# Optimization experiments

Measured on AMD Instinct MI355X. Metric: run time of the kernel, lower is better.

Reference implementation:

```python
import jax, jax.numpy as jnp
import numpy as np

L = 2048          # memory_length
NB = 512          # attn_num_basis
HID = 1024        # n_heads * head_dim
H = 16            # n_heads
D = 64            # head_dim
B = 8             # batch
QLEN = 2048
RIDGE = 0.5
SIGMAS = np.array([0.005, 0.01], dtype=np.float64)


def _build_basis_and_G():
    # torch.meshgrid(linspace(0,1,NB//2), sigmas) with 'ij' indexing, then flatten:
    mu_lin = np.linspace(0.0, 1.0, NB // len(SIGMAS))
    basis_mu = np.repeat(mu_lin, len(SIGMAS))          # [NB]
    basis_sigma = np.tile(SIGMAS, NB // len(SIGMAS))   # [NB]
    # get_positions with padding, even memory_length:
    shift = 1.0 / (2.0 * L)
    pos = np.linspace(-0.5 + shift, 1.5 - shift, 2 * L)  # [2L]
    # F[j, p] = N(pos_p; mu_j, sigma_j^2)
    F = np.exp(-0.5 * ((pos[None, :] - basis_mu[:, None]) / basis_sigma[:, None]) ** 2) \
        / (basis_sigma[:, None] * np.sqrt(2.0 * np.pi))  # [NB, 2L]
    G = F.T @ np.linalg.inv(F @ F.T + RIDGE * np.eye(NB))  # [2L, NB]
    Gs = G[L // 2: -(L // 2)]                              # [L, NB]
    return (basis_mu.astype(np.float32), basis_sigma.astype(np.float32),
            Gs.astype(np.float32))


def setup_inputs() -> dict:
    key = jax.random.key(0)
    ks = jax.random.split(key, 10)
    basis_mu, basis_sigma, Gs = _build_basis_and_G()
    inp = {
        "k": jax.random.normal(ks[0], (B, L, HID), jnp.float32),
        "query": jax.random.normal(ks[1], (B, H, QLEN, D), jnp.float32),
        "W_mask": jax.random.normal(ks[2], (L, L), jnp.float32) * (L ** -0.5),
        "b_mask": jnp.zeros((L,), jnp.float32),
        "Wq": jax.random.normal(ks[3], (HID, HID), jnp.float32) * (HID ** -0.5),
        "Wk": jax.random.normal(ks[4], (HID, HID), jnp.float32) * (HID ** -0.5),
        "Wv": jax.random.normal(ks[5], (HID, HID), jnp.float32) * (HID ** -0.5),
        "Wo": jax.random.normal(ks[6], (HID, HID), jnp.float32) * (HID ** -0.5),
        "w_mu": jax.random.normal(ks[7], (NB,), jnp.float32) * (NB ** -0.5),
        "w_sigma": jax.random.normal(ks[8], (NB,), jnp.float32) * (NB ** -0.5),
        "Gs": jnp.asarray(Gs),
        "basis_mu": jnp.asarray(basis_mu),
        "basis_sigma": jnp.asarray(basis_sigma),
    }
    return inp


def reference(k, query, W_mask, b_mask, Wq, Wk, Wv, Wo, w_mu, w_sigma,
              Gs, basis_mu, basis_sigma):
    b, l, hid = k.shape
    _, h, q, d = query.shape
    # k -> [B, hid, L]; affine mask over memory-length dim + sigmoid gate
    km = jnp.swapaxes(k, 1, 2)
    reg_mask = jax.nn.sigmoid(jnp.einsum('bhl,ml->bhm', km, W_mask) + b_mask)
    km = km * reg_mask
    # value_function: B = (k @ Gs).permute(0,2,1) -> [B, NB, hid]
    Bmat = jnp.einsum('bhl,ln->bnh', km, Gs)
    keys = (Bmat @ Wk.T).reshape(b, -1, h, d).transpose(0, 2, 1, 3)   # [B,H,NB,d]
    vals = (Bmat @ Wv.T).reshape(b, -1, h, d).transpose(0, 2, 1, 3)   # [B,H,NB,d]
    qh = (query.transpose(0, 2, 1, 3).reshape(b, q, hid) @ Wq.T)
    qh = qh.reshape(b, q, h, d).transpose(0, 2, 1, 3)                 # [B,H,q,d]
    # score: q / sqrt(head_dim) @ keys^T -> [B,H,q,NB]
    scores = jnp.einsum('bhqd,bhnd->bhqn', qh / jnp.sqrt(jnp.float32(d)), keys)
    # affine mu / sigma^2 of the continuous attention Gaussian
    mu = jax.nn.sigmoid(scores @ w_mu)[..., None]                      # [B,H,q,1]
    sigma_sq = jnp.maximum(jax.nn.softplus(scores @ w_sigma), 1e-6)[..., None]
    # ContinuousSoftmax with Gaussian basis: r_j = E_{t~N(mu,sig^2)}[psi_j(t)]
    #                                            = N(mu_j; mu, sig^2 + sigma_j^2)
    var = sigma_sq + basis_sigma ** 2                                  # [B,H,q,NB]
    r = jnp.exp(-0.5 * (mu - basis_mu) ** 2 / var) / jnp.sqrt(2.0 * jnp.pi * var)
    ctx = jnp.einsum('bhqn,bhnd->bqhd', r, vals).reshape(b, q, hid)
    return ctx @ Wo.T
```

## Files before the change

### kernel.cpp

```cpp
#include <hip/hip_runtime.h>
#include <hip/hip_bf16.h>

#define L_   2048
#define NB_  512
#define HID_ 1024
#define H_   16
#define D_   64
#define B_   8
#define Q_   2048

typedef unsigned short u16;
typedef float  f32x4  __attribute__((ext_vector_type(4)));
typedef short  short8 __attribute__((ext_vector_type(8)));

__device__ __forceinline__ u16 f2b_e22(float x) {
    __hip_bfloat16 h = __float2bfloat16(x);
    union { __hip_bfloat16 h; u16 u; } cv; cv.h = h; return cv.u;
}
__device__ __forceinline__ float b2f_e22(u16 u) {
    union { u16 u; __hip_bfloat16 h; } cv; cv.u = u; return __bfloat162float(cv.h);
}
__device__ __forceinline__ float ldin_e22(const void* p, long i, int bf) {
    return bf ? b2f_e22(((const u16*)p)[i]) : ((const float*)p)[i];
}

#define GLDSE22(gp, lp) __builtin_amdgcn_global_load_lds( \
    (const __attribute__((address_space(1))) void*)(gp), \
    (__attribute__((address_space(3))) void*)(lp), 16, 0, 0)

__global__ void probe_e22(const unsigned* __restrict__ k, int* __restrict__ flag)
{
    __shared__ int cnt;
    if (threadIdx.x == 0) cnt = 0;
    __syncthreads();
    int c = 0;
    for (int i = threadIdx.x; i < 4096; i += 256) {
        unsigned e = (k[i] >> 7) & 0xFFu;
        if (e >= 100u && e <= 135u) c++;
    }
    atomicAdd(&cnt, c);
    __syncthreads();
    if (threadIdx.x == 0) *flag = (cnt > 2048) ? 1 : 0;
}

__global__ void beacon_e22(float* __restrict__ out, long n, float code)
{
    long i = (long)blockIdx.x * blockDim.x + threadIdx.x;
    long st = (long)gridDim.x * blockDim.x;
    for (; i < n; i += st) out[i] = 0.f;
    if (blockIdx.x == 0 && threadIdx.x == 0) out[0] = code;
}

__global__ void conv_e22(const void* __restrict__ in, u16* __restrict__ out,
                         long n, const int* __restrict__ dflag)
{
    const int bf = *dflag;
    long i = (long)blockIdx.x * blockDim.x + threadIdx.x;
    long st = (long)gridDim.x * blockDim.x;
    for (; i < n; i += st) out[i] = f2b_e22(ldin_e22(in, i, bf));
}

__global__ void qg_e22(const void* __restrict__ q, u16* __restrict__ out,
                       const int* __restrict__ dflag)
{
    const int bf = *dflag;
    const long n = (long)B_ * H_ * Q_ * D_;
    long i = (long)blockIdx.x * blockDim.x + threadIdx.x;
    long st = (long)gridDim.x * blockDim.x;
    for (; i < n; i += st) {
        long dd = i & 63; long t = i >> 6;
        long qq = t & (Q_ - 1); t >>= 11;
        long h = t & (H_ - 1); long b = t >> 4;
        out[(b * Q_ + qq) * HID_ + h * 64 + dd] = f2b_e22(ldin_e22(q, i, bf));
    }
}

__global__ void split_e22(const float* __restrict__ in, u16* __restrict__ hi,
                          u16* __restrict__ lo, long n)
{
    long i = (long)blockIdx.x * blockDim.x + threadIdx.x;
    long st = (long)gridDim.x * blockDim.x;
    for (; i < n; i += st) {
        float v = in[i];
        u16 h = f2b_e22(v);
        hi[i] = h;
        lo[i] = f2b_e22(v - b2f_e22(h));
    }
}

__global__ __launch_bounds__(256)
void tr_e22(const void* __restrict__ in, u16* __restrict__ out,
            int R, int C, long sIn, long sOut, const int* __restrict__ dflag)
{
    const int bf = *dflag;
    __shared__ u16 t[64][66];
    const long ibase = (long)blockIdx.z * sIn;
    u16* ob = out + (long)blockIdx.z * sOut;
    const int r0 = blockIdx.y * 64, c0 = blockIdx.x * 64;
    const int lc = threadIdx.x & 63, rb = threadIdx.x >> 6;
    #pragma unroll
    for (int kk = 0; kk < 16; ++kk) {
        int r = rb * 16 + kk;
        t[r][lc] = f2b_e22(ldin_e22(in, ibase + (long)(r0 + r) * C + c0 + lc, bf));
    }
    __syncthreads();
    #pragma unroll
    for (int kk = 0; kk < 16; ++kk) {
        int cr = rb * 16 + kk;
        ob[(long)(c0 + cr) * R + r0 + lc] = t[lc][cr];
    }
}

__global__ void ew_e22(float* __restrict__ S, const u16* __restrict__ kT,
                       const void* __restrict__ bmask, const int* __restrict__ dflag)
{
    const int bf = *dflag;
    const long n = (long)B_ * HID_ * L_;
    long i = (long)blockIdx.x * blockDim.x + threadIdx.x;
    long st = (long)gridDim.x * blockDim.x;
    for (; i < n; i += st) {
        long m = i & (L_ - 1);
        float sg = 1.f / (1.f + expf(-(S[i] + ldin_e22(bmask, m, bf))));
        S[i] = b2f_e22(kT[i]) * sg;
    }
}

__global__ __launch_bounds__(256)
void gemm_e22(const u16* __restrict__ A, int lda, long sA,
              const u16* __restrict__ Bt, int ldb, long sB,
              float* __restrict__ Cv, int ldc, long sC, int K,
              float scale, int epi)
{
    __shared__ u16 As[128 * 32];
    __shared__ u16 Bs[128 * 32];
    const int tid = threadIdx.x;
    const int wv = tid >> 6, ln = tid & 63;
    const int g = ln >> 4, lr = ln & 15;
    const int wr = wv >> 1, wc = wv & 1;
    const int bm = blockIdx.y * 128, bn = blockIdx.x * 128;
    const u16* Ab = A + (long)blockIdx.z * sA;
    const u16* Bb = Bt + (long)blockIdx.z * sB;

    const int sr = ln >> 2;
    const int scl = (ln & 3) * 8;
    const u16* ga0 = Ab + (long)(bm + wv * 16 + sr) * lda + scl;
    const u16* ga1 = Ab + (long)(bm + (wv + 4) * 16 + sr) * lda + scl;
    const u16* gb0 = Bb + (long)(bn + wv * 16 + sr) * ldb + scl;
    const u16* gb1 = Bb + (long)(bn + (wv + 4) * 16 + sr) * ldb + scl;
    u16* la0 = &As[wv * 512];
    u16* la1 = &As[(wv + 4) * 512];
    u16* lb0 = &Bs[wv * 512];
    u16* lb1 = &Bs[(wv + 4) * 512];

    f32x4 acc[4][4];
    #pragma unroll
    for (int i = 0; i < 4; ++i)
        #pragma unroll
        for (int j = 0; j < 4; ++j) acc[i][j] = (f32x4){0.f, 0.f, 0.f, 0.f};

    for (int k0 = 0; k0 < K; k0 += 32) {
        GLDSE22(ga0 + k0, la0);
        GLDSE22(ga1 + k0, la1);
        GLDSE22(gb0 + k0, lb0);
        GLDSE22(gb1 + k0, lb1);
        __syncthreads();
        short8 af[4], bfr[4];
        #pragma unroll
        for (int i = 0; i < 4; ++i) af[i] = *(const short8*)&As[(wr * 64 + i * 16 + lr) * 32 + g * 8];
        #pragma unroll
        for (int j = 0; j < 4; ++j) bfr[j] = *(const short8*)&Bs[(wc * 64 + j * 16 + lr) * 32 + g * 8];
        #pragma unroll
        for (int i = 0; i < 4; ++i)
            #pragma unroll
            for (int j = 0; j < 4; ++j)
                acc[i][j] = __builtin_amdgcn_mfma_f32_16x16x32_bf16(af[i], bfr[j], acc[i][j], 0, 0, 0);
        __syncthreads();
    }

    const int r0 = bm + wr * 64 + g * 4;
    const int c0 = bn + wc * 64 + lr;
    float* C = Cv + (long)blockIdx.z * sC;
    #pragma unroll
    for (int i = 0; i < 4; ++i)
        #pragma unroll
        for (int j = 0; j < 4; ++j)
            #pragma unroll
            for (int r = 0; r < 4; ++r) {
                long o = (long)(r0 + i * 16 + r) * ldc + (c0 + j * 16);
                if (epi == 4) C[o] += acc[i][j][r];
                else          C[o] = scale * acc[i][j][r];
            }
}

__global__ __launch_bounds__(256)
void sg2c_e22(const float* __restrict__ kmF, const void* __restrict__ gs,
              float* __restrict__ BmatF, const int* __restrict__ dflag)
{
    const int bf = *dflag;
    __shared__ float gst[32][65];
    __shared__ float kmt[64][33];
    const int b = blockIdx.z;
    const int c0 = blockIdx.x * 64, n0 = blockIdx.y * 64;
    const int tid = threadIdx.x;
    const int tx = tid & 15, ty = tid >> 4;
    float acc[4][4];
    #pragma unroll
    for (int i = 0; i < 4; ++i)
        #pragma unroll
        for (int j = 0; j < 4; ++j) acc[i][j] = 0.f;

    const int glc = tid & 63, grb = tid >> 6;
    const int klc = tid & 31, krb = tid >> 5;
    for (int l0 = 0; l0 < L_; l0 += 32) {
        #pragma unroll
        for (int kk = 0; kk < 8; ++kk) {
            int r = grb + 4 * kk;
            gst[r][glc] = ldin_e22(gs, (long)(l0 + r) * NB_ + n0 + glc, bf);
            int rr = krb + 8 * kk;
            kmt[rr][klc] = kmF[((long)b * HID_ + c0 + rr) * L_ + l0 + klc];
        }
        __syncthreads();
        #pragma unroll 8
        for (int kk = 0; kk < 32; ++kk) {
            float gv[4], kv[4];
            #pragma unroll
            for (int j = 0; j < 4; ++j) gv[j] = gst[kk][ty + 16 * j];
            #pragma unroll
            for (int i = 0; i < 4; ++i) kv[i] = kmt[tx + 16 * i][kk];
            #pragma unroll
            for (int i = 0; i < 4; ++i)
                #pragma unroll
                for (int j = 0; j < 4; ++j)
                    acc[i][j] += kv[i] * gv[j];
        }
        __syncthreads();
    }
    #pragma unroll
    for (int j = 0; j < 4; ++j)
        #pragma unroll
        for (int i = 0; i < 4; ++i)
            BmatF[((long)b * NB_ + n0 + ty + 16 * j) * HID_ + c0 + tx + 16 * i] = acc[i][j];
}

__global__ void kw_e22(const float* __restrict__ keysF,
                       const void* __restrict__ w_mu, const void* __restrict__ w_sg,
                       float* __restrict__ kwmu, float* __restrict__ kwsg,
                       const int* __restrict__ dflag)
{
    const int bf = *dflag;
    const int bh = blockIdx.x;
    const int b = bh >> 4, h = bh & 15;
    const int d = threadIdx.x;
    const float* kb = keysF + (long)b * NB_ * HID_ + h * 64 + d;
    float am = 0.f, as = 0.f;
    for (int n = 0; n < NB_; ++n) {
        float kv = kb[(long)n * HID_];
        am += ldin_e22(w_mu, n, bf) * kv;
        as += ldin_e22(w_sg, n, bf) * kv;
    }
    kwmu[(long)bh * 64 + d] = am;
    kwsg[(long)bh * 64 + d] = as;
}

__global__ __launch_bounds__(256)
void attn_e22(float* __restrict__ qh, const float* __restrict__ valsF,
              const float* __restrict__ kwmu, const float* __restrict__ kwsg,
              const void* __restrict__ bmu, const void* __restrict__ bsg,
              const int* __restrict__ dflag)
{
    const int bf = *dflag;
    __shared__ float bmuS[512], bvS[512];
    __shared__ float rST[512][16];
    const int b = blockIdx.z, h = blockIdx.y;
    const int tid = threadIdx.x, wv = tid >> 6, lane = tid & 63;

    for (int i = tid; i < 512; i += 256) {
        bmuS[i] = ldin_e22(bmu, i, bf);
        float s = ldin_e22(bsg, i, bf);
        bvS[i] = s * s;
    }
    __syncthreads();

    const int q0 = blockIdx.x * 16 + wv * 4;
    const float km = kwmu[((long)b * H_ + h) * 64 + lane];
    const float ks = kwsg[((long)b * H_ + h) * 64 + lane];

    float qv[4], mu[4], sq[4];
    float* qrow[4];
    #pragma unroll
    for (int j = 0; j < 4; ++j) {
        qrow[j] = qh + ((long)b * Q_ + q0 + j) * HID_ + h * 64;
        qv[j] = qrow[j][lane];
        float pm = qv[j] * km, ps = qv[j] * ks;
        #pragma unroll
        for (int off = 32; off > 0; off >>= 1) {
            pm += __shfl_xor(pm, off);
            ps += __shfl_xor(ps, off);
        }
        mu[j] = 1.f / (1.f + expf(-pm));
        float sp = (ps > 0.f) ? (ps + log1pf(expf(-ps))) : log1pf(expf(ps));
        sq[j] = fmaxf(sp, 1e-6f);
    }

    #pragma unroll
    for (int j = 0; j < 4; ++j) {
        #pragma unroll
        for (int jj = 0; jj < 8; ++jj) {
            int n = lane + 64 * jj;
            float var = sq[j] + bvS[n];
            float dd = mu[j] - bmuS[n];
            rST[n][wv * 4 + j] = expf(-0.5f * dd * dd / var)
                                 / sqrtf(6.283185307179586f * var);
        }
    }
    __syncthreads();

    const float* vb = valsF + (long)b * NB_ * HID_ + h * 64 + lane;
    float cd[4] = {0.f, 0.f, 0.f, 0.f};
    for (int n = 0; n < 512; ++n) {
        float v = vb[(long)n * HID_];
        const f32x4 r4 = *(const f32x4*)&rST[n][wv * 4];
        #pragma unroll
        for (int j = 0; j < 4; ++j)
            cd[j] += r4[j] * v;
    }
    #pragma unroll
    for (int j = 0; j < 4; ++j)
        qrow[j][lane] = cd[j];
}

extern "C" void kernel_launch(void* const* d_in, const int* in_sizes, int n_in,
                              void* d_out, int out_size, void* d_ws, size_t ws_size,
                              hipStream_t stream)
{
    static const int SZ_INS[13] = {16777216,16777216,4194304,2048,1048576,1048576,
                                   1048576,1048576,512,512,1048576,512,512};
    bool mi = (n_in == 13);
    if (mi) for (int i = 0; i < 13; ++i) if (in_sizes[i] != SZ_INS[i]) { mi = false; break; }
    if (!mi) {
        beacon_e22<<<2048, 256, 0, stream>>>((float*)d_out, (long)out_size, 7777777.f);
        return;
    }

    const void* k_in  = d_in[0];
    const void* query = d_in[1];
    const void* wm_f  = d_in[2];
    const void* bmask = d_in[3];
    const void* wq_f  = d_in[4];
    const void* wk_f  = d_in[5];
    const void* wv_f  = d_in[6];
    const void* wo_f  = d_in[7];
    const void* w_mu  = d_in[8];
    const void* w_sg  = d_in[9];
    const void* gs_f  = d_in[10];
    const void* bmu   = d_in[11];
    const void* bsg   = d_in[12];

    char* ws = (char*)d_ws;
    size_t off = 0;
    auto alloc = [&](size_t bytes) { char* p = ws + off; off += (bytes + 255) & ~(size_t)255; return p; };
    const size_t MiB = 1048576;
    const long SBH = (long)NB_ * HID_;
    const long SQH = (long)Q_ * HID_;
    const long SHL = (long)HID_ * L_;
    int*   dflag = (int*)alloc(256);
    char*  RQ    = alloc(64 * MiB);
    char*  SC    = alloc(64 * MiB);
    char*  BK    = alloc(16 * MiB);
    float* valsF = (float*)alloc(16 * MiB);
    u16*   wqc   = (u16*)alloc((size_t)HID_ * HID_ * 2);
    u16*   wkc   = (u16*)alloc((size_t)HID_ * HID_ * 2);
    u16*   wvc   = (u16*)alloc((size_t)HID_ * HID_ * 2);
    float* kwmu  = (float*)alloc((size_t)B_ * H_ * 64 * 4);
    float* kwsg  = (float*)alloc((size_t)B_ * H_ * 64 * 4);
    if (ws_size < off) {
        beacon_e22<<<2048, 256, 0, stream>>>((float*)d_out, (long)out_size, 9999999.f);
        return;
    }
    u16*   wmask = (u16*)RQ;
    u16*   kTp   = (u16*)(RQ + 8 * MiB);
    float* qhF   = (float*)RQ;
    float* ctxF  = qhF;
    float* SCf   = (float*)SC;
    u16*   qflat = (u16*)SC;
    u16*   bmh   = (u16*)(SC + 32 * MiB);
    u16*   bml   = (u16*)(SC + 40 * MiB);
    u16*   ctxh  = (u16*)SC;
    u16*   ctxl  = (u16*)(SC + 32 * MiB);
    float* BmatF = (float*)BK;
    float* keysF = (float*)BK;
    u16*   woc   = (u16*)valsF;

    probe_e22<<<1, 256, 0, stream>>>((const unsigned*)k_in, dflag);
    conv_e22<<<1024, 256, 0, stream>>>(wq_f, wqc, (long)HID_ * HID_, dflag);
    conv_e22<<<1024, 256, 0, stream>>>(wk_f, wkc, (long)HID_ * HID_, dflag);
    conv_e22<<<1024, 256, 0, stream>>>(wv_f, wvc, (long)HID_ * HID_, dflag);
    conv_e22<<<2048, 256, 0, stream>>>(wm_f, wmask, (long)L_ * L_, dflag);
    tr_e22<<<dim3(HID_ / 64, L_ / 64, B_), 256, 0, stream>>>(
        k_in, kTp, L_, HID_, (long)L_ * HID_, SHL, dflag);

    gemm_e22<<<dim3(L_ / 128, HID_ / 128, B_), 256, 0, stream>>>(
        kTp, L_, SHL, wmask, L_, 0, SCf, L_, SHL, L_, 1.f, 3);
    ew_e22<<<2048, 256, 0, stream>>>(SCf, kTp, bmask, dflag);

    sg2c_e22<<<dim3(HID_ / 64, NB_ / 64, B_), 256, 0, stream>>>(SCf, gs_f, BmatF, dflag);
    split_e22<<<2048, 256, 0, stream>>>(BmatF, bmh, bml, (long)B_ * SBH);

    qg_e22<<<4096, 256, 0, stream>>>(query, qflat, dflag);
    gemm_e22<<<dim3(HID_ / 128, Q_ / 128, B_), 256, 0, stream>>>(
        qflat, HID_, SQH, wqc, HID_, 0, qhF, HID_, SQH, HID_, 0.125f, 3);

    gemm_e22<<<dim3(HID_ / 128, NB_ / 128, B_), 256, 0, stream>>>(
        bmh, HID_, SBH, wkc, HID_, 0, keysF, HID_, SBH, HID_, 1.f, 3);
    gemm_e22<<<dim3(HID_ / 128, NB_ / 128, B_), 256, 0, stream>>>(
        bml, HID_, SBH, wkc, HID_, 0, keysF, HID_, SBH, HID_, 1.f, 4);
    kw_e22<<<B_ * H_, 64, 0, stream>>>(keysF, w_mu, w_sg, kwmu, kwsg, dflag);

    gemm_e22<<<dim3(HID_ / 128, NB_ / 128, B_), 256, 0, stream>>>(
        bmh, HID_, SBH, wvc, HID_, 0, valsF, HID_, SBH, HID_, 1.f, 3);
    gemm_e22<<<dim3(HID_ / 128, NB_ / 128, B_), 256, 0, stream>>>(
        bml, HID_, SBH, wvc, HID_, 0, valsF, HID_, SBH, HID_, 1.f, 4);

    attn_e22<<<dim3(Q_ / 16, H_, B_), 256, 0, stream>>>(
        qhF, valsF, kwmu, kwsg, bmu, bsg, dflag);

    conv_e22<<<1024, 256, 0, stream>>>(wo_f, woc, (long)HID_ * HID_, dflag);
    split_e22<<<2048, 256, 0, stream>>>(ctxF, ctxh, ctxl, (long)B_ * SQH);
    gemm_e22<<<dim3(HID_ / 128, Q_ / 128, B_), 256, 0, stream>>>(
        ctxh, HID_, SQH, woc, HID_, 0, (float*)d_out, HID_, SQH, HID_, 1.f, 3);
    gemm_e22<<<dim3(HID_ / 128, Q_ / 128, B_), 256, 0, stream>>>(
        ctxl, HID_, SQH, woc, HID_, 0, (float*)d_out, HID_, SQH, HID_, 1.f, 4);
}
```

Before: 1.592 ms.

## Move attention context contraction onto bf16 MFMA with split-precision operands

The attention kernel's r·V contraction, previously a scalar FP32 loop over 512 basis functions per lane, now runs on 16x16x32 bf16 MFMA. Both the r weights and the values are split into hi/lo bf16 pairs, and three MFMAs per step recover near-FP32 accuracy. A new transpose-and-split kernel lays out values as [B, HID, NB] hi/lo bf16 so tiles can be staged in LDS. The goal is to cut the scalar FMA and strided global-load cost of the attention stage, at the price of an extra kernel launch, extra LDS syncs and bf16 truncation error.

```diff
diff --git a/kernel.cpp b/kernel.cpp
--- a/kernel.cpp
+++ b/kernel.cpp
@@ -13,22 +13,22 @@
 typedef float  f32x4  __attribute__((ext_vector_type(4)));
 typedef short  short8 __attribute__((ext_vector_type(8)));
 
-__device__ __forceinline__ u16 f2b_e22(float x) {
+__device__ __forceinline__ u16 f2b_g24(float x) {
     __hip_bfloat16 h = __float2bfloat16(x);
     union { __hip_bfloat16 h; u16 u; } cv; cv.h = h; return cv.u;
 }
-__device__ __forceinline__ float b2f_e22(u16 u) {
+__device__ __forceinline__ float b2f_g24(u16 u) {
     union { u16 u; __hip_bfloat16 h; } cv; cv.u = u; return __bfloat162float(cv.h);
 }
-__device__ __forceinline__ float ldin_e22(const void* p, long i, int bf) {
-    return bf ? b2f_e22(((const u16*)p)[i]) : ((const float*)p)[i];
-}
-
-#define GLDSE22(gp, lp) __builtin_amdgcn_global_load_lds( \
+__device__ __forceinline__ float ldin_g24(const void* p, long i, int bf) {
+    return bf ? b2f_g24(((const u16*)p)[i]) : ((const float*)p)[i];
+}
+
+#define GLDSG24(gp, lp) __builtin_amdgcn_global_load_lds( \
     (const __attribute__((address_space(1))) void*)(gp), \
     (__attribute__((address_space(3))) void*)(lp), 16, 0, 0)
 
-__global__ void probe_e22(const unsigned* __restrict__ k, int* __restrict__ flag)
+__global__ void probe_g24(const unsigned* __restrict__ k, int* __restrict__ flag)
 {
     __shared__ int cnt;
     if (threadIdx.x == 0) cnt = 0;
@@ -43,7 +43,7 @@
     if (threadIdx.x == 0) *flag = (cnt > 2048) ? 1 : 0;
 }
 
-__global__ void beacon_e22(float* __restrict__ out, long n, float code)
+__global__ void beacon_g24(float* __restrict__ out, long n, float code)
 {
     long i = (long)blockIdx.x * blockDim.x + threadIdx.x;
     long st = (long)gridDim.x * blockDim.x;
@@ -51,16 +51,16 @@
     if (blockIdx.x == 0 && threadIdx.x == 0) out[0] = code;
 }
 
-__global__ void conv_e22(const void* __restrict__ in, u16* __restrict__ out,
+__global__ void conv_g24(const void* __restrict__ in, u16* __restrict__ out,
                          long n, const int* __restrict__ dflag)
 {
     const int bf = *dflag;
     long i = (long)blockIdx.x * blockDim.x + threadIdx.x;
     long st = (long)gridDim.x * blockDim.x;
-    for (; i < n; i += st) out[i] = f2b_e22(ldin_e22(in, i, bf));
-}
-
-__global__ void qg_e22(const void* __restrict__ q, u16* __restrict__ out,
+    for (; i < n; i += st) out[i] = f2b_g24(ldin_g24(in, i, bf));
+}
+
+__global__ void qg_g24(const void* __restrict__ q, u16* __restrict__ out,
                        const int* __restrict__ dflag)
 {
     const int bf = *dflag;
@@ -71,25 +71,25 @@
         long dd = i & 63; long t = i >> 6;
         long qq = t & (Q_ - 1); t >>= 11;
         long h = t & (H_ - 1); long b = t >> 4;
-        out[(b * Q_ + qq) * HID_ + h * 64 + dd] = f2b_e22(ldin_e22(q, i, bf));
-    }
-}
-
-__global__ void split_e22(const float* __restrict__ in, u16* __restrict__ hi,
+        out[(b * Q_ + qq) * HID_ + h * 64 + dd] = f2b_g24(ldin_g24(q, i, bf));
+    }
+}
+
+__global__ void split_g24(const float* __restrict__ in, u16* __restrict__ hi,
                           u16* __restrict__ lo, long n)
 {
     long i = (long)blockIdx.x * blockDim.x + threadIdx.x;
     long st = (long)gridDim.x * blockDim.x;
     for (; i < n; i += st) {
         float v = in[i];
-        u16 h = f2b_e22(v);
+        u16 h = f2b_g24(v);
         hi[i] = h;
-        lo[i] = f2b_e22(v - b2f_e22(h));
+        lo[i] = f2b_g24(v - b2f_g24(h));
     }
 }
 
 __global__ __launch_bounds__(256)
-void tr_e22(const void* __restrict__ in, u16* __restrict__ out,
+void tr_g24(const void* __restrict__ in, u16* __restrict__ out,
             int R, int C, long sIn, long sOut, const int* __restrict__ dflag)
 {
     const int bf = *dflag;
@@ -101,7 +101,7 @@
     #pragma unroll
     for (int kk = 0; kk < 16; ++kk) {
         int r = rb * 16 + kk;
-        t[r][lc] = f2b_e22(ldin_e22(in, ibase + (long)(r0 + r) * C + c0 + lc, bf));
+        t[r][lc] = f2b_g24(ldin_g24(in, ibase + (long)(r0 + r) * C + c0 + lc, bf));
     }
     __syncthreads();
     #pragma unroll
@@ -111,7 +111,34 @@
     }
 }
 
-__global__ void ew_e22(float* __restrict__ S, const u16* __restrict__ kT,
+__global__ __launch_bounds__(256)
+void trsplitv_g24(const float* __restrict__ in, u16* __restrict__ hi,
+                  u16* __restrict__ lo, int R, int C, long sIn, long sOut)
+{
+    __shared__ float t[64][65];
+    const float* ib = in + (long)blockIdx.z * sIn;
+    u16* oh = hi + (long)blockIdx.z * sOut;
+    u16* ol = lo + (long)blockIdx.z * sOut;
+    const int r0 = blockIdx.y * 64, c0 = blockIdx.x * 64;
+    const int lc = threadIdx.x & 63, rb = threadIdx.x >> 6;
+    #pragma unroll
+    for (int kk = 0; kk < 16; ++kk) {
+        int r = rb * 16 + kk;
+        t[r][lc] = ib[(long)(r0 + r) * C + c0 + lc];
+    }
+    __syncthreads();
+    #pragma unroll
+    for (int kk = 0; kk < 16; ++kk) {
+        int cr = rb * 16 + kk;
+        float v = t[lc][cr];
+        u16 hh = f2b_g24(v);
+        long o = (long)(c0 + cr) * R + r0 + lc;
+        oh[o] = hh;
+        ol[o] = f2b_g24(v - b2f_g24(hh));
+    }
+}
+
+__global__ void ew_g24(float* __restrict__ S, const u16* __restrict__ kT,
                        const void* __restrict__ bmask, const int* __restrict__ dflag)
 {
     const int bf = *dflag;
@@ -120,13 +147,13 @@
     long st = (long)gridDim.x * blockDim.x;
     for (; i < n; i += st) {
         long m = i & (L_ - 1);
-        float sg = 1.f / (1.f + expf(-(S[i] + ldin_e22(bmask, m, bf))));
-        S[i] = b2f_e22(kT[i]) * sg;
+        float sg = 1.f / (1.f + expf(-(S[i] + ldin_g24(bmask, m, bf))));
+        S[i] = b2f_g24(kT[i]) * sg;
     }
 }
 
 __global__ __launch_bounds__(256)
-void gemm_e22(const u16* __restrict__ A, int lda, long sA,
+void gemm_g24(const u16* __restrict__ A, int lda, long sA,
               const u16* __restrict__ Bt, int ldb, long sB,
               float* __restrict__ Cv, int ldc, long sC, int K,
               float scale, int epi)
@@ -159,10 +186,10 @@
         for (int j = 0; j < 4; ++j) acc[i][j] = (f32x4){0.f, 0.f, 0.f, 0.f};
 
     for (int k0 = 0; k0 < K; k0 += 32) {
-        GLDSE22(ga0 + k0, la0);
-        GLDSE22(ga1 + k0, la1);
-        GLDSE22(gb0 + k0, lb0);
-        GLDSE22(gb1 + k0, lb1);
+        GLDSG24(ga0 + k0, la0);
+        GLDSG24(ga1 + k0, la1);
+        GLDSG24(gb0 + k0, lb0);
+        GLDSG24(gb1 + k0, lb1);
         __syncthreads();
         short8 af[4], bfr[4];
         #pragma unroll
@@ -193,7 +220,7 @@
 }
 
 __global__ __launch_bounds__(256)
-void sg2c_e22(const float* __restrict__ kmF, const void* __restrict__ gs,
+void sg2c_g24(const float* __restrict__ kmF, const void* __restrict__ gs,
               float* __restrict__ BmatF, const int* __restrict__ dflag)
 {
     const int bf = *dflag;
@@ -215,7 +242,7 @@
         #pragma unroll
         for (int kk = 0; kk < 8; ++kk) {
             int r = grb + 4 * kk;
-            gst[r][glc] = ldin_e22(gs, (long)(l0 + r) * NB_ + n0 + glc, bf);
+            gst[r][glc] = ldin_g24(gs, (long)(l0 + r) * NB_ + n0 + glc, bf);
             int rr = krb + 8 * kk;
             kmt[rr][klc] = kmF[((long)b * HID_ + c0 + rr) * L_ + l0 + klc];
         }
@@ -242,7 +269,7 @@
             BmatF[((long)b * NB_ + n0 + ty + 16 * j) * HID_ + c0 + tx + 16 * i] = acc[i][j];
 }
 
-__global__ void kw_e22(const float* __restrict__ keysF,
+__global__ void kw_g24(const float* __restrict__ keysF,
                        const void* __restrict__ w_mu, const void* __restrict__ w_sg,
                        float* __restrict__ kwmu, float* __restrict__ kwsg,
                        const int* __restrict__ dflag)
@@ -255,78 +282,102 @@
     float am = 0.f, as = 0.f;
     for (int n = 0; n < NB_; ++n) {
         float kv = kb[(long)n * HID_];
-        am += ldin_e22(w_mu, n, bf) * kv;
-        as += ldin_e22(w_sg, n, bf) * kv;
+        am += ldin_g24(w_mu, n, bf) * kv;
+        as += ldin_g24(w_sg, n, bf) * kv;
     }
     kwmu[(long)bh * 64 + d] = am;
     kwsg[(long)bh * 64 + d] = as;
 }
 
 __global__ __launch_bounds__(256)
-void attn_e22(float* __restrict__ qh, const float* __restrict__ valsF,
+void attn_g24(float* __restrict__ qh,
+              const u16* __restrict__ vTh, const u16* __restrict__ vTl,
               const float* __restrict__ kwmu, const float* __restrict__ kwsg,
               const void* __restrict__ bmu, const void* __restrict__ bsg,
               const int* __restrict__ dflag)
 {
     const int bf = *dflag;
     __shared__ float bmuS[512], bvS[512];
-    __shared__ float rST[512][16];
+    __shared__ float mu_s[16], sq_s[16];
+    __shared__ u16 rAh[16 * 80], rAl[16 * 80];
+    __shared__ u16 vBh[64 * 80], vBl[64 * 80];
     const int b = blockIdx.z, h = blockIdx.y;
     const int tid = threadIdx.x, wv = tid >> 6, lane = tid & 63;
+    const int qbase = blockIdx.x * 16;
 
     for (int i = tid; i < 512; i += 256) {
-        bmuS[i] = ldin_e22(bmu, i, bf);
-        float s = ldin_e22(bsg, i, bf);
+        bmuS[i] = ldin_g24(bmu, i, bf);
+        float s = ldin_g24(bsg, i, bf);
         bvS[i] = s * s;
     }
-    __syncthreads();
-
-    const int q0 = blockIdx.x * 16 + wv * 4;
+
     const float km = kwmu[((long)b * H_ + h) * 64 + lane];
     const float ks = kwsg[((long)b * H_ + h) * 64 + lane];
 
-    float qv[4], mu[4], sq[4];
-    float* qrow[4];
     #pragma unroll
     for (int j = 0; j < 4; ++j) {
-        qrow[j] = qh + ((long)b * Q_ + q0 + j) * HID_ + h * 64;
-        qv[j] = qrow[j][lane];
-        float pm = qv[j] * km, ps = qv[j] * ks;
+        const float* qrow = qh + ((long)b * Q_ + qbase + wv * 4 + j) * HID_ + h * 64;
+        float qv = qrow[lane];
+        float pm = qv * km, ps = qv * ks;
         #pragma unroll
         for (int off = 32; off > 0; off >>= 1) {
             pm += __shfl_xor(pm, off);
             ps += __shfl_xor(ps, off);
         }
-        mu[j] = 1.f / (1.f + expf(-pm));
-        float sp = (ps > 0.f) ? (ps + log1pf(expf(-ps))) : log1pf(expf(ps));
-        sq[j] = fmaxf(sp, 1e-6f);
-    }
-
-    #pragma unroll
-    for (int j = 0; j < 4; ++j) {
-        #pragma unroll
-        for (int jj = 0; jj < 8; ++jj) {
-            int n = lane + 64 * jj;
-            float var = sq[j] + bvS[n];
-            float dd = mu[j] - bmuS[n];
-            rST[n][wv * 4 + j] = expf(-0.5f * dd * dd / var)
-                                 / sqrtf(6.283185307179586f * var);
+        if (lane == 0) {
+            mu_s[wv * 4 + j] = 1.f / (1.f + expf(-pm));
+            float sp = (ps > 0.f) ? (ps + log1pf(expf(-ps))) : log1pf(expf(ps));
+            sq_s[wv * 4 + j] = fmaxf(sp, 1e-6f);
         }
     }
     __syncthreads();
 
-    const float* vb = valsF + (long)b * NB_ * HID_ + h * 64 + lane;
-    float cd[4] = {0.f, 0.f, 0.f, 0.f};
-    for (int n = 0; n < 512; ++n) {
-        float v = vb[(long)n * HID_];
-        const f32x4 r4 = *(const f32x4*)&rST[n][wv * 4];
-        #pragma unroll
-        for (int j = 0; j < 4; ++j)
-            cd[j] += r4[j] * v;
-    }
-    #pragma unroll
-    for (int j = 0; j < 4; ++j)
-        qrow[j][lane] = cd[j];
+    const int rrow = tid >> 4;
+    const int rn0  = (tid & 15) * 4;
+    const float muR = mu_s[rrow], sqR = sq_s[rrow];
+    const int g = lane >> 4, lr = lane & 15;
+    f32x4 acc = (f32x4){0.f, 0.f, 0.f, 0.f};
+
+    for (int kt = 0; kt < 8; ++kt) {
+        const int nbase = kt * 64;
+        #pragma unroll
+        for (int i = 0; i < 4; ++i) {
+            int n = rn0 + i;
+            int N = nbase + n;
+            float var = sqR + bvS[N];
+            float dd = muR - bmuS[N];
+            float rv = expf(-0.5f * dd * dd / var) * rsqrtf(6.2831853071795864f * var);
+            u16 hh = f2b_g24(rv);
+            rAh[rrow * 80 + n] = hh;
+            rAl[rrow * 80 + n] = f2b_g24(rv - b2f_g24(hh));
+        }
+        #pragma unroll
+        for (int j2 = 0; j2 < 2; ++j2) {
+            int id = tid * 2 + j2;
+            int d = id >> 3, nb8 = id & 7;
+            long go = ((long)b * HID_ + h * 64 + d) * NB_ + nbase + nb8 * 8;
+            *(short8*)&vBh[d * 80 + nb8 * 8] = *(const short8*)(vTh + go);
+            *(short8*)&vBl[d * 80 + nb8 * 8] = *(const short8*)(vTl + go);
+        }
+        __syncthreads();
+        #pragma unroll
+        for (int kss = 0; kss < 2; ++kss) {
+            short8 ah = *(const short8*)&rAh[lr * 80 + kss * 32 + g * 8];
+            short8 al = *(const short8*)&rAl[lr * 80 + kss * 32 + g * 8];
+            short8 bh = *(const short8*)&vBh[(wv * 16 + lr) * 80 + kss * 32 + g * 8];
+            short8 bl = *(const short8*)&vBl[(wv * 16 + lr) * 80 + kss * 32 + g * 8];
+            acc = __builtin_amdgcn_mfma_f32_16x16x32_bf16(ah, bh, acc, 0, 0, 0);
+            acc = __builtin_amdgcn_mfma_f32_16x16x32_bf16(ah, bl, acc, 0, 0, 0);
+            acc = __builtin_amdgcn_mfma_f32_16x16x32_bf16(al, bh, acc, 0, 0, 0);
+        }
+        __syncthreads();
+    }
+
+    #pragma unroll
+    for (int r = 0; r < 4; ++r) {
+        int row = g * 4 + r;
+        qh[((long)b * Q_ + qbase + row) * HID_ + h * 64 + wv * 16 + lr] = acc[r];
+    }
 }
 
 extern "C" void kernel_launch(void* const* d_in, const int* in_sizes, int n_in,
@@ -338,7 +389,7 @@
     bool mi = (n_in == 13);
     if (mi) for (int i = 0; i < 13; ++i) if (in_sizes[i] != SZ_INS[i]) { mi = false; break; }
     if (!mi) {
-        beacon_e22<<<2048, 256, 0, stream>>>((float*)d_out, (long)out_size, 7777777.f);
+        beacon_g24<<<2048, 256, 0, stream>>>((float*)d_out, (long)out_size, 7777777.f);
         return;
     }
 
@@ -374,7 +425,7 @@
     float* kwmu  = (float*)alloc((size_t)B_ * H_ * 64 * 4);
     float* kwsg  = (float*)alloc((size_t)B_ * H_ * 64 * 4);
     if (ws_size < off) {
-        beacon_e22<<<2048, 256, 0, stream>>>((float*)d_out, (long)out_size, 9999999.f);
+        beacon_g24<<<2048, 256, 0, stream>>>((float*)d_out, (long)out_size, 9999999.f);
         return;
     }
     u16*   wmask = (u16*)RQ;
@@ -389,45 +440,50 @@
     u16*   ctxl  = (u16*)(SC + 32 * MiB);
     float* BmatF = (float*)BK;
     float* keysF = (float*)BK;
+    u16*   vTh   = (u16*)BK;
+    u16*   vTl   = (u16*)(BK + 8 * MiB);
     u16*   woc   = (u16*)valsF;
 
-    probe_e22<<<1, 256, 0, stream>>>((const unsigned*)k_in, dflag);
-    conv_e22<<<1024, 256, 0, stream>>>(wq_f, wqc, (long)HID_ * HID_, dflag);
-    conv_e22<<<1024, 256, 0, stream>>>(wk_f, wkc, (long)HID_ * HID_, dflag);
-    conv_e22<<<1024, 256, 0, stream>>>(wv_f, wvc, (long)HID_ * HID_, dflag);
-    conv_e22<<<2048, 256, 0, stream>>>(wm_f, wmask, (long)L_ * L_, dflag);
-    tr_e22<<<dim3(HID_ / 64, L_ / 64, B_), 256, 0, stream>>>(
+    probe_g24<<<1, 256, 0, stream>>>((const unsigned*)k_in, dflag);
+    conv_g24<<<1024, 256, 0, stream>>>(wq_f, wqc, (long)HID_ * HID_, dflag);
+    conv_g24<<<1024, 256, 0, stream>>>(wk_f, wkc, (long)HID_ * HID_, dflag);
+    conv_g24<<<1024, 256, 0, stream>>>(wv_f, wvc, (long)HID_ * HID_, dflag);
+    conv_g24<<<2048, 256, 0, stream>>>(wm_f, wmask, (long)L_ * L_, dflag);
+    tr_g24<<<dim3(HID_ / 64, L_ / 64, B_), 256, 0, stream>>>(
         k_in, kTp, L_, HID_, (long)L_ * HID_, SHL, dflag);
 
-    gemm_e22<<<dim3(L_ / 128, HID_ / 128, B_), 256, 0, stream>>>(
+    gemm_g24<<<dim3(L_ / 128, HID_ / 128, B_), 256, 0, stream>>>(
         kTp, L_, SHL, wmask, L_, 0, SCf, L_, SHL, L_, 1.f, 3);
-    ew_e22<<<2048, 256, 0, stream>>>(SCf, kTp, bmask, dflag);
-
-    sg2c_e22<<<dim3(HID_ / 64, NB_ / 64, B_), 256, 0, stream>>>(SCf, gs_f, BmatF, dflag);
-    split_e22<<<2048, 256, 0, stream>>>(BmatF, bmh, bml, (long)B_ * SBH);
-
-    qg_e22<<<4096, 256, 0, stream>>>(query, qflat, dflag);
-    gemm_e22<<<dim3(HID_ / 128, Q_ / 128, B_), 256, 0, stream>>>(
+    ew_g24<<<2048, 256, 0, stream>>>(SCf, kTp, bmask, dflag);
+
+    sg2c_g24<<<dim3(HID_ / 64, NB_ / 64, B_), 256, 0, stream>>>(SCf, gs_f, BmatF, dflag);
+    split_g24<<<2048, 256, 0, stream>>>(BmatF, bmh, bml, (long)B_ * SBH);
+
+    qg_g24<<<4096, 256, 0, stream>>>(query, qflat, dflag);
+    gemm_g24<<<dim3(HID_ / 128, Q_ / 128, B_), 256, 0, stream>>>(
         qflat, HID_, SQH, wqc, HID_, 0, qhF, HID_, SQH, HID_, 0.125f, 3);
 
-    gemm_e22<<<dim3(HID_ / 128, NB_ / 128, B_), 256, 0, stream>>>(
+    gemm_g24<<<dim3(HID_ / 128, NB_ / 128, B_), 256, 0, stream>>>(
         bmh, HID_, SBH, wkc, HID_, 0, keysF, HID_, SBH, HID_, 1.f, 3);
-    gemm_e22<<<dim3(HID_ / 128, NB_ / 128, B_), 256, 0, stream>>>(
+    gemm_g24<<<dim3(HID_ / 128, NB_ / 128, B_), 256, 0, stream>>>(
         bml, HID_, SBH, wkc, HID_, 0, keysF, HID_, SBH, HID_, 1.f, 4);
-    kw_e22<<<B_ * H_, 64, 0, stream>>>(keysF, w_mu, w_sg, kwmu, kwsg, dflag);
-
-    gemm_e22<<<dim3(HID_ / 128, NB_ / 128, B_), 256, 0, stream>>>(
+    kw_g24<<<B_ * H_, 64, 0, stream>>>(keysF, w_mu, w_sg, kwmu, kwsg, dflag);
+
+    gemm_g24<<<dim3(HID_ / 128, NB_ / 128, B_), 256, 0, stream>>>(
         bmh, HID_, SBH, wvc, HID_, 0, valsF, HID_, SBH, HID_, 1.f, 3);
-    gemm_e22<<<dim3(HID_ / 128, NB_ / 128, B_), 256, 0, stream>>>(
+    gemm_g24<<<dim3(HID_ / 128, NB_ / 128, B_), 256, 0, stream>>>(
         bml, HID_, SBH, wvc, HID_, 0, valsF, HID_, SBH, HID_, 1.f, 4);
 
-    attn_e22<<<dim3(Q_ / 16, H_, B_), 256, 0, stream>>>(
-        qhF, valsF, kwmu, kwsg, bmu, bsg, dflag);
-
-    conv_e22<<<1024, 256, 0, stream>>>(wo_f, woc, (long)HID_ * HID_, dflag);
-    split_e22<<<2048, 256, 0, stream>>>(ctxF, ctxh, ctxl, (long)B_ * SQH);
-    gemm_e22<<<dim3(HID_ / 128, Q_ / 128, B_), 256, 0, stream>>>(
+    trsplitv_g24<<<dim3(HID_ / 64, NB_ / 64, B_), 256, 0, stream>>>(
+        valsF, vTh, vTl, NB_, HID_, SBH, SBH);
+
+    attn_g24<<<dim3(Q_ / 16, H_, B_), 256, 0, stream>>>(
+        qhF, vTh, vTl, kwmu, kwsg, bmu, bsg, dflag);
+
+    conv_g24<<<1024, 256, 0, stream>>>(wo_f, woc, (long)HID_ * HID_, dflag);
+    split_g24<<<2048, 256, 0, stream>>>(ctxF, ctxh, ctxl, (long)B_ * SQH);
+    gemm_g24<<<dim3(HID_ / 128, Q_ / 128, B_), 256, 0, stream>>>(
         ctxh, HID_, SQH, woc, HID_, 0, (float*)d_out, HID_, SQH, HID_, 1.f, 3);
-    gemm_e22<<<dim3(HID_ / 128, Q_ / 128, B_), 256, 0, stream>>>(
+    gemm_g24<<<dim3(HID_ / 128, Q_ / 128, B_), 256, 0, stream>>>(
         ctxl, HID_, SQH, woc, HID_, 0, (float*)d_out, HID_, SQH, HID_, 1.f, 4);
 }
```

Result: faster. 1.326 ms (-16.7%).
